# Kernel tuning notes

Hardware: AMD Instinct MI355X
Metric: run time of the kernel (lower is better)

## Reference

```python
import jax, jax.numpy as jnp
import numpy as np

V, H, B, T = 32000, 1024, 32, 256  # vocab, rnn_size, batch, seq_length


def setup_inputs() -> dict:
    key = jax.random.key(0)
    ks = jax.random.split(key, 6)
    s = 1.0 / np.sqrt(H)
    return {
        "input_data": jax.random.randint(ks[0], (B, T), 0, V, dtype=jnp.int32),
        "targets": jax.random.randint(ks[1], (B, T), 0, V, dtype=jnp.int32),
        "embedding": jax.random.uniform(ks[2], (V, H), minval=-1.0, maxval=1.0, dtype=jnp.float32),
        "softmax_b": jnp.zeros((V,), jnp.float32),
        "W0": (jax.random.normal(ks[3], (2 * H, 4 * H)) * s).astype(jnp.float32),
        "b0": jnp.zeros((4 * H,), jnp.float32),
        "W1": (jax.random.normal(ks[4], (2 * H, 4 * H)) * s).astype(jnp.float32),
        "b1": jnp.zeros((4 * H,), jnp.float32),
    }


def _lstm_step(x, c, h, W, b):
    # TF LSTMCell: gates i, j, f, o; forget_bias = 1.0
    z = jnp.concatenate([x, h], axis=-1) @ W + b  # [B, 4H]
    i, j, f, o = jnp.split(z, 4, axis=-1)
    c2 = c * jax.nn.sigmoid(f + 1.0) + jax.nn.sigmoid(i) * jnp.tanh(j)
    h2 = jax.nn.sigmoid(o) * jnp.tanh(c2)
    return c2, h2


def reference(input_data, targets, embedding, softmax_b, W0, b0, W1, b1):
    x = embedding[input_data]  # [B, T, H]
    Bb, Hh = x.shape[0], embedding.shape[1]
    zeros = jnp.zeros((Bb, Hh), x.dtype)
    init = ((zeros, zeros), (zeros, zeros))  # ((c0,h0),(c1,h1))

    def step(carry, xt):
        (c0, h0), (c1, h1) = carry
        c0, h0 = _lstm_step(xt, c0, h0, W0, b0)
        c1, h1 = _lstm_step(h0, c1, h1, W1, b1)
        return ((c0, h0), (c1, h1)), h1

    _, outs = jax.lax.scan(step, init, jnp.swapaxes(x, 0, 1))  # [T, B, H]
    output = jnp.swapaxes(outs, 0, 1).reshape(-1, Hh)  # [B*T, H]
    logits = output @ embedding.T + softmax_b  # tied softmax weights, [B*T, V]
    labels = targets.reshape(-1)
    logp = jax.nn.log_softmax(logits)
    loss = -jnp.take_along_axis(logp, labels[:, None], axis=1)[:, 0]
    cost = jnp.sum(loss) / Bb
    return logits, cost
```

## Files before the change

kernel.cpp:

```cpp
#include <hip/hip_runtime.h>
#include <hip/hip_bf16.h>

#define DEV static __device__ __forceinline__

typedef unsigned short u16;
typedef unsigned long long u64;
typedef __attribute__((ext_vector_type(8))) short short8;
typedef __attribute__((ext_vector_type(4))) float f32x4;

constexpr int V = 32000, H = 1024, B = 32, T = 256;
constexpr int BT = B * T;
constexpr int G  = 4 * H;
constexpr int NCH = V / 128;
constexpr int NWG2 = 256;
constexpr int RSTRIDE = 32 * 2048 + 2048;

constexpr size_t SZ_WT    = (size_t)G * 2048 * 2;
constexpr size_t OFF_W0T  = 0;
constexpr size_t OFF_W1T  = OFF_W0T + SZ_WT;
constexpr size_t OFF_EBF  = OFF_W1T + SZ_WT;
constexpr size_t OFF_XBF  = OFF_EBF + (size_t)V * H * 2;
constexpr size_t OFF_XP0  = OFF_XBF + (size_t)BT * H * 2;
constexpr size_t OFF_H1   = OFF_XP0 + (size_t)BT * G * 2;
constexpr size_t OFF_HSEQ = OFF_H1 + (size_t)BT * H * 2;
constexpr size_t SZ_HSEQ  = (size_t)(T + 2) * RSTRIDE * 2;
constexpr size_t OFF_SYNC = OFF_HSEQ + SZ_HSEQ;
constexpr size_t OFF_PMAX = OFF_SYNC + 8192;
constexpr size_t OFF_PSUM = OFF_PMAX + (size_t)BT * NCH * 4;
constexpr size_t OFF_LOSS = OFF_PSUM + (size_t)BT * NCH * 4;

DEV u16 f2bf(float x) {
  union { float f; unsigned int u; } v; v.f = x;
  unsigned int r = v.u + 0x7fffu + ((v.u >> 16) & 1u);
  return (u16)(r >> 16);
}
DEV float bf2f(u16 b) {
  union { unsigned int u; float f; } v; v.u = ((unsigned int)b) << 16;
  return v.f;
}
DEV float sigm(float x) { return 1.f / (1.f + expf(-x)); }

DEV void gload_lds16(const u16* g, u16* l) {
  __builtin_amdgcn_global_load_lds(
      (__attribute__((address_space(1))) void*)g,
      (__attribute__((address_space(3))) void*)l, 16, 0, 0);
}


__global__ void k_transpose_cvt(const float* __restrict__ in, u16* __restrict__ out,
                                int R, int C) {
  __shared__ float tile[32][33];
  int bc = blockIdx.x * 32, br = blockIdx.y * 32;
  int tx = threadIdx.x & 31, ty0 = threadIdx.x >> 5;
#pragma unroll
  for (int i = 0; i < 4; ++i) {
    int ty = ty0 + i * 8;
    tile[ty][tx] = in[(size_t)(br + ty) * C + bc + tx];
  }
  __syncthreads();
#pragma unroll
  for (int i = 0; i < 4; ++i) {
    int ty = ty0 + i * 8;
    out[(size_t)(bc + ty) * R + br + tx] = f2bf(tile[tx][ty]);
  }
}

__global__ void k_cvt_bf16(const float* __restrict__ in, u16* __restrict__ out, int n4) {
  int i = blockIdx.x * blockDim.x + threadIdx.x;
  int stride = gridDim.x * blockDim.x;
  for (; i < n4; i += stride) {
    float4 v = ((const float4*)in)[i];
    ushort4 o;
    o.x = f2bf(v.x); o.y = f2bf(v.y); o.z = f2bf(v.z); o.w = f2bf(v.w);
    ((ushort4*)out)[i] = o;
  }
}

__global__ void k_gather_x(const float* __restrict__ emb, const int* __restrict__ inp,
                           u16* __restrict__ Xbf) {
  int row = blockIdx.x;
  int t = row >> 5, b = row & 31;
  int tok = inp[b * T + t];
  const float4* src = (const float4*)(emb + (size_t)tok * H);
  ushort4* dst = (ushort4*)(Xbf + (size_t)row * H);
  float4 v = src[threadIdx.x];
  ushort4 o;
  o.x = f2bf(v.x); o.y = f2bf(v.y); o.z = f2bf(v.z); o.w = f2bf(v.w);
  dst[threadIdx.x] = o;
}

__global__ void k_zero(unsigned int* __restrict__ p, int nwords) {
  int i = blockIdx.x * blockDim.x + threadIdx.x;
  int stride = gridDim.x * blockDim.x;
  for (; i < nwords; i += stride) p[i] = 0u;
}

template <bool SM_EPI, int CMODE>
__global__ __launch_bounds__(256)
void k_gemm(const u16* __restrict__ A, int lda,
            const u16* __restrict__ Bt, int ldb,
            float* __restrict__ C, int ldc,
            const float* __restrict__ bias, int K,
            float* __restrict__ pmax, float* __restrict__ psum, int nch) {
  __shared__ alignas(16) u16 ldsA[128 * 32];
  __shared__ alignas(16) u16 ldsB[128 * 32];
  __shared__ float2 red[128][2];

  unsigned nwg = gridDim.x * gridDim.y;
  unsigned flat = blockIdx.y * gridDim.x + blockIdx.x;
  unsigned nf = (flat & 7) * (nwg >> 3) + (flat >> 3);
  unsigned bx = nf % gridDim.x, by = nf / gridDim.x;

  int tid = threadIdx.x, lane = tid & 63, w = tid >> 6;
  int row0 = by * 128, col0 = bx * 128;
  int wr = w >> 1, wc = w & 1;
  int c15 = lane & 15, q4 = lane >> 4;

  const u16* ag[2]; const u16* bg[2];
#pragma unroll
  for (int j = 0; j < 2; ++j) {
    int r = (j * 4 + w) * 16 + (lane >> 2);
    int k = (lane & 3) * 8;
    ag[j] = A + (size_t)(row0 + r) * lda + k;
    bg[j] = Bt + (size_t)(col0 + r) * ldb + k;
  }
  u16* lA0 = ldsA + (size_t)(0 + w) * 512;
  u16* lA1 = ldsA + (size_t)(4 + w) * 512;
  u16* lB0 = ldsB + (size_t)(0 + w) * 512;
  u16* lB1 = ldsB + (size_t)(4 + w) * 512;

  f32x4 acc[4][4];
#pragma unroll
  for (int m = 0; m < 4; ++m)
#pragma unroll
    for (int n = 0; n < 4; ++n) acc[m][n] = (f32x4){0.f, 0.f, 0.f, 0.f};

  int nk = K >> 5;
  for (int kk = 0; kk < nk; ++kk) {
    int kb = kk * 32;
    gload_lds16(ag[0] + kb, lA0);
    gload_lds16(ag[1] + kb, lA1);
    gload_lds16(bg[0] + kb, lB0);
    gload_lds16(bg[1] + kb, lB1);
    __syncthreads();

    short8 af[4], bfr[4];
#pragma unroll
    for (int m = 0; m < 4; ++m)
      af[m] = *(const short8*)(ldsA + (wr * 64 + m * 16 + c15) * 32 + q4 * 8);
#pragma unroll
    for (int n = 0; n < 4; ++n)
      bfr[n] = *(const short8*)(ldsB + (wc * 64 + n * 16 + c15) * 32 + q4 * 8);
#pragma unroll
    for (int m = 0; m < 4; ++m)
#pragma unroll
      for (int n = 0; n < 4; ++n)
        acc[m][n] = __builtin_amdgcn_mfma_f32_16x16x32_bf16(af[m], bfr[n], acc[m][n], 0, 0, 0);
    __syncthreads();
  }

  float bias_n[4];
#pragma unroll
  for (int n = 0; n < 4; ++n) bias_n[n] = bias[col0 + wc * 64 + n * 16 + c15];

#pragma unroll
  for (int m = 0; m < 4; ++m) {
#pragma unroll
    for (int jr = 0; jr < 4; ++jr) {
      int r_g = row0 + wr * 64 + m * 16 + q4 * 4 + jr;
      float v[4];
#pragma unroll
      for (int n = 0; n < 4; ++n) {
        int c_g = col0 + wc * 64 + n * 16 + c15;
        float val = acc[m][n][jr] + bias_n[n];
        if (CMODE == 0) {
          C[(size_t)r_g * ldc + c_g] = val;
        } else {
          int tt = r_g >> 5, bb = r_g & 31;
          int q = c_g >> 10, wgup = (c_g & 1023) >> 3, uu = c_g & 7;
          ((u16*)C)[((((size_t)tt * 128 + wgup) * 32 + bb) * 32) + q * 8 + uu] = f2bf(val);
        }
        v[n] = val;
      }
      if (SM_EPI) {
        float mx = fmaxf(fmaxf(v[0], v[1]), fmaxf(v[2], v[3]));
        float s = __expf(v[0] - mx) + __expf(v[1] - mx) + __expf(v[2] - mx) + __expf(v[3] - mx);
#pragma unroll
        for (int d = 1; d < 16; d <<= 1) {
          float mo = __shfl_xor(mx, d, 64);
          float so = __shfl_xor(s, d, 64);
          float M2 = fmaxf(mx, mo);
          s = s * __expf(mx - M2) + so * __expf(mo - M2);
          mx = M2;
        }
        if (c15 == 0) red[wr * 64 + m * 16 + q4 * 4 + jr][wc] = make_float2(mx, s);
      }
    }
  }
  if (SM_EPI) {
    __syncthreads();
    if (tid < 128) {
      float2 a = red[tid][0], b2 = red[tid][1];
      float M2 = fmaxf(a.x, b2.x);
      float S = a.y * __expf(a.x - M2) + b2.y * __expf(b2.x - M2);
      pmax[(size_t)(row0 + tid) * nch + bx] = M2;
      psum[(size_t)(row0 + tid) * nch + bx] = S;
    }
  }
}


#define RED(w_, bt_, nt_, r_, c_) red[((((w_)*2 + (bt_)) * 2 + (nt_)) * 16 + (r_)) * 16 + (c_)]

DEV void bar_sync(int* __restrict__ cnt, int target) {
  __syncthreads();
  if (threadIdx.x == 0) {
    __hip_atomic_fetch_add(cnt, 1, __ATOMIC_RELAXED, __HIP_MEMORY_SCOPE_AGENT);
    while (__hip_atomic_load(cnt, __ATOMIC_RELAXED, __HIP_MEMORY_SCOPE_AGENT) < target)
      __builtin_amdgcn_s_sleep(4);
  }
  __builtin_amdgcn_sched_barrier(0);
  __syncthreads();
}

DEV void epoch_wait(const int* __restrict__ cnt, int target) {
  if (threadIdx.x == 0) {
    while (__hip_atomic_load(cnt, __ATOMIC_RELAXED, __HIP_MEMORY_SCOPE_AGENT) < target)
      __builtin_amdgcn_s_sleep(4);
  }
  __builtin_amdgcn_sched_barrier(0);
  __syncthreads();
}

template <int KH, bool IS_L0>
DEV void lstm_role(const u16* __restrict__ WT,
                   const u16* __restrict__ xp0p,
                   const float* __restrict__ zb1,
                   u16* __restrict__ hseq, u16* __restrict__ H1bf,
                   int* __restrict__ c_own, int* __restrict__ c_epoch,
                   float* __restrict__ red, int wgu) {
  constexpr int KOFF = IS_L0 ? 1024 : 0;
  constexpr int KS = KH / 4;
  constexpr int NKC = KS / 32;
  int tid = threadIdx.x, lane = tid & 63, w = tid >> 6;
  int c15 = lane & 15, q4 = lane >> 4;
  int eb = tid >> 3, eu = tid & 7;

  short8 wfr[2][NKC];
#pragma unroll
  for (int nt = 0; nt < 2; ++nt) {
    int lr = nt * 16 + c15;
    const u16* rp = WT + (size_t)((lr >> 3) * 1024 + wgu * 8 + (lr & 7)) * 2048
                    + KOFF + w * KS + q4 * 8;
#pragma unroll
    for (int kc = 0; kc < NKC; ++kc)
      wfr[nt][kc] = *(const short8*)(rp + kc * 32);
  }

  float zpc[4];
  if (!IS_L0) {
#pragma unroll
    for (int q = 0; q < 4; ++q) zpc[q] = zb1[q * 1024 + wgu * 8 + eu];
  }
  float creg = 0.f;

  for (int it_t = 0; it_t < T; ++it_t) {
    int t = IS_L0 ? it_t : it_t + 1;

    if (!IS_L0) epoch_wait(c_epoch, 128 * t);

    float zp[4];
    if (IS_L0) {
#pragma unroll
      for (int q = 0; q < 4; ++q)
        zp[q] = bf2f(xp0p[((((size_t)t * 128 + wgu) * 32 + eb) * 32) + q * 8 + eu]);
    } else {
#pragma unroll
      for (int q = 0; q < 4; ++q) zp[q] = zpc[q];
    }

    const u16* hread = hseq + (size_t)t * RSTRIDE;
    f32x4 acc[2][2];
#pragma unroll
    for (int bt = 0; bt < 2; ++bt)
#pragma unroll
      for (int nt = 0; nt < 2; ++nt) acc[bt][nt] = (f32x4){0.f, 0.f, 0.f, 0.f};

#pragma unroll
    for (int kc = 0; kc < NKC; ++kc) {
      int kh = w * KS + kc * 32 + q4 * 8;
      short8 a0 = *(const short8*)(hread + (size_t)c15 * 2048 + kh);
      short8 a1 = *(const short8*)(hread + (size_t)(16 + c15) * 2048 + kh);
      acc[0][0] = __builtin_amdgcn_mfma_f32_16x16x32_bf16(a0, wfr[0][kc], acc[0][0], 0, 0, 0);
      acc[0][1] = __builtin_amdgcn_mfma_f32_16x16x32_bf16(a0, wfr[1][kc], acc[0][1], 0, 0, 0);
      acc[1][0] = __builtin_amdgcn_mfma_f32_16x16x32_bf16(a1, wfr[0][kc], acc[1][0], 0, 0, 0);
      acc[1][1] = __builtin_amdgcn_mfma_f32_16x16x32_bf16(a1, wfr[1][kc], acc[1][1], 0, 0, 0);
    }

#pragma unroll
    for (int bt = 0; bt < 2; ++bt)
#pragma unroll
      for (int nt = 0; nt < 2; ++nt)
#pragma unroll
        for (int jr = 0; jr < 4; ++jr)
          RED(w, bt, nt, q4 * 4 + jr, c15) = acc[bt][nt][jr];
    __syncthreads();

    int bt = eb >> 4, rr = eb & 15;
    float z[4];
#pragma unroll
    for (int q = 0; q < 4; ++q) {
      int lr = q * 8 + eu, nt = lr >> 4, cc = lr & 15;
      z[q] = RED(0, bt, nt, rr, cc) + RED(1, bt, nt, rr, cc) +
             RED(2, bt, nt, rr, cc) + RED(3, bt, nt, rr, cc) + zp[q];
    }
    float gi = sigm(z[0]);
    float gj = tanhf(z[1]);
    float gf = sigm(z[2] + 1.f);
    float go = sigm(z[3]);
    creg = creg * gf + gi * gj;
    float hv = go * tanhf(creg);

    int hb = (int)f2bf(hv);
    int hp = __shfl_xor(hb, 1, 64);
    if (!(tid & 1)) {
      unsigned int pack = (unsigned int)(u16)hb | ((unsigned int)(u16)hp << 16);
      u16* hwr = hseq + (size_t)(t + 1) * RSTRIDE + (IS_L0 ? 0 : 1024);
      __hip_atomic_store((unsigned int*)(hwr + (size_t)eb * 2048 + wgu * 8 + eu), pack,
                         __ATOMIC_RELAXED, __HIP_MEMORY_SCOPE_AGENT);
      if (!IS_L0)
        *(unsigned int*)(H1bf + ((size_t)eb * T + (t - 1)) * H + wgu * 8 + eu) = pack;
    }

    bar_sync(c_own, 128 * (IS_L0 ? t + 1 : t));
  }
}

__global__ __launch_bounds__(256, 1)
void k_lstm_persistent(const u16* __restrict__ W0T, const u16* __restrict__ W1T,
                       const u16* __restrict__ xp0p, const float* __restrict__ b1,
                       u16* __restrict__ hseq, u16* __restrict__ H1bf,
                       int* __restrict__ sync) {
  __shared__ float red[4 * 2 * 2 * 16 * 16];
  int wg = blockIdx.x;
  if (wg < 128)
    lstm_role<1024, true>(W0T, xp0p, nullptr, hseq, H1bf, sync, nullptr, red, wg);
  else
    lstm_role<2048, false>(W1T, nullptr, b1, hseq, H1bf, sync + 64, sync, red, wg - 128);
}

__global__ void k_rowfin(const float* __restrict__ pmax, const float* __restrict__ psum,
                         const float* __restrict__ Cl, const int* __restrict__ targets,
                         float* __restrict__ loss) {
  int row = blockIdx.x;
  int tid = threadIdx.x, lane = tid & 63, w = tid >> 6;
  float mx = -1e30f, s = 0.f;
  if (tid < NCH) { mx = pmax[(size_t)row * NCH + tid]; s = psum[(size_t)row * NCH + tid]; }
#pragma unroll
  for (int d = 1; d < 64; d <<= 1) {
    float mo = __shfl_xor(mx, d, 64);
    float so = __shfl_xor(s, d, 64);
    float M2 = fmaxf(mx, mo);
    s = s * __expf(mx - M2) + so * __expf(mo - M2);
    mx = M2;
  }
  __shared__ float2 wred[4];
  if (lane == 0) wred[w] = make_float2(mx, s);
  __syncthreads();
  if (tid == 0) {
    float M = wred[0].x, S = wred[0].y;
#pragma unroll
    for (int i = 1; i < 4; ++i) {
      float M2 = fmaxf(M, wred[i].x);
      S = S * __expf(M - M2) + wred[i].y * __expf(wred[i].x - M2);
      M = M2;
    }
    float logZ = M + logf(S);
    int tgt = targets[row];
    float xt = Cl[(size_t)row * V + tgt];
    loss[row] = logZ - xt;
  }
}

__global__ void k_cost(const float* __restrict__ loss, float* __restrict__ out) {
  int tid = threadIdx.x, lane = tid & 63, w = tid >> 6;
  float s = 0.f;
  for (int i = tid; i < BT; i += 256) s += loss[i];
#pragma unroll
  for (int d = 1; d < 64; d <<= 1) s += __shfl_xor(s, d, 64);
  __shared__ float ws4[4];
  if (lane == 0) ws4[w] = s;
  __syncthreads();
  if (tid == 0) out[0] = (ws4[0] + ws4[1] + ws4[2] + ws4[3]) * (1.0f / B);
}

extern "C" void kernel_launch(void* const* d_in, const int* in_sizes, int n_in,
                              void* d_out, int out_size, void* d_ws, size_t ws_size,
                              hipStream_t stream) {
  const int*   input_data = (const int*)d_in[0];
  const int*   targets    = (const int*)d_in[1];
  const float* emb        = (const float*)d_in[2];
  const float* softmax_b  = (const float*)d_in[3];
  const float* W0         = (const float*)d_in[4];
  const float* b0         = (const float*)d_in[5];
  const float* W1         = (const float*)d_in[6];
  const float* b1         = (const float*)d_in[7];
  float* out = (float*)d_out;
  char*  ws  = (char*)d_ws;

  u16*   W0T  = (u16*)(ws + OFF_W0T);
  u16*   W1T  = (u16*)(ws + OFF_W1T);
  u16*   Ebf  = (u16*)(ws + OFF_EBF);
  u16*   Xbf  = (u16*)(ws + OFF_XBF);
  u16*   xp0p = (u16*)(ws + OFF_XP0);
  u16*   H1bf = (u16*)(ws + OFF_H1);
  u16*   hseq = (u16*)(ws + OFF_HSEQ);
  int*   sync = (int*)(ws + OFF_SYNC);
  float* pmax = (float*)(ws + OFF_PMAX);
  float* psum = (float*)(ws + OFF_PSUM);
  float* lossb= (float*)(ws + OFF_LOSS);

  k_transpose_cvt<<<dim3(G / 32, 2048 / 32), 256, 0, stream>>>(W0, W0T, 2048, G);
  k_transpose_cvt<<<dim3(G / 32, 2048 / 32), 256, 0, stream>>>(W1, W1T, 2048, G);
  k_cvt_bf16<<<2048, 256, 0, stream>>>(emb, Ebf, V * H / 4);
  k_gather_x<<<BT, 256, 0, stream>>>(emb, input_data, Xbf);
  k_zero<<<64, 256, 0, stream>>>((unsigned int*)(ws + OFF_HSEQ), RSTRIDE);
  k_zero<<<1, 256, 0, stream>>>((unsigned int*)(ws + OFF_SYNC), 2048);

  k_gemm<false, 1><<<dim3(G / 128, BT / 128), 256, 0, stream>>>(
      Xbf, H, W0T, 2048, (float*)xp0p, G, b0, H, nullptr, nullptr, 0);

  k_lstm_persistent<<<dim3(NWG2), dim3(256), 0, stream>>>(
      W0T, W1T, xp0p, b1, hseq, H1bf, sync);

  k_gemm<true, 0><<<dim3(V / 128, BT / 128), 256, 0, stream>>>(
      H1bf, H, Ebf, H, out, V, softmax_b, H, pmax, psum, NCH);

  k_rowfin<<<BT, 256, 0, stream>>>(pmax, psum, out, targets, lossb);
  k_cost<<<1, 256, 0, stream>>>(lossb, out + (size_t)BT * V);
}
```

Baseline: 3.190 ms.

## Replace atomic counter barriers with per-timestep per-workgroup flag arrays in LSTM

Replaces the shared atomic-add counter barriers in the persistent LSTM kernel with per-timestep, per-workgroup ready flags. Each workgroup publishes its own flag with a plain store after writing h, and consumers poll 128 flags in parallel with one wavefront. Layer 1 now waits only on the layer-0 flags for step t-1 and its own layer's flags for t-2, which removes atomic contention on a single counter and loosens the layer coupling. The cost is a larger flag buffer that must be zeroed each run, and it relies on relaxed-ordering visibility of the h stores before the flag.

```diff
diff --git a/kernel.cpp b/kernel.cpp
--- a/kernel.cpp
+++ b/kernel.cpp
@@ -25,7 +25,8 @@
 constexpr size_t OFF_HSEQ = OFF_H1 + (size_t)BT * H * 2;
 constexpr size_t SZ_HSEQ  = (size_t)(T + 2) * RSTRIDE * 2;
 constexpr size_t OFF_SYNC = OFF_HSEQ + SZ_HSEQ;
-constexpr size_t OFF_PMAX = OFF_SYNC + 8192;
+constexpr size_t SZ_SYNC  = (size_t)2 * 256 * 128 * 4;
+constexpr size_t OFF_PMAX = OFF_SYNC + SZ_SYNC;
 constexpr size_t OFF_PSUM = OFF_PMAX + (size_t)BT * NCH * 4;
 constexpr size_t OFF_LOSS = OFF_PSUM + (size_t)BT * NCH * 4;
 
@@ -212,24 +213,33 @@
 
 #define RED(w_, bt_, nt_, r_, c_) red[((((w_)*2 + (bt_)) * 2 + (nt_)) * 16 + (r_)) * 16 + (c_)]
 
-DEV void bar_sync(int* __restrict__ cnt, int target) {
-  __syncthreads();
-  if (threadIdx.x == 0) {
-    __hip_atomic_fetch_add(cnt, 1, __ATOMIC_RELAXED, __HIP_MEMORY_SCOPE_AGENT);
-    while (__hip_atomic_load(cnt, __ATOMIC_RELAXED, __HIP_MEMORY_SCOPE_AGENT) < target)
-      __builtin_amdgcn_s_sleep(4);
+DEV void wait_flags(const int* __restrict__ fa, const int* __restrict__ fb) {
+  if (threadIdx.x < 64) {
+    int lane = threadIdx.x;
+    while (true) {
+      int ok = 1;
+      if (fa) {
+        int a0 = __hip_atomic_load(fa + lane,      __ATOMIC_RELAXED, __HIP_MEMORY_SCOPE_AGENT);
+        int a1 = __hip_atomic_load(fa + 64 + lane, __ATOMIC_RELAXED, __HIP_MEMORY_SCOPE_AGENT);
+        ok &= (a0 != 0) & (a1 != 0);
+      }
+      if (fb) {
+        int b0 = __hip_atomic_load(fb + lane,      __ATOMIC_RELAXED, __HIP_MEMORY_SCOPE_AGENT);
+        int b1 = __hip_atomic_load(fb + 64 + lane, __ATOMIC_RELAXED, __HIP_MEMORY_SCOPE_AGENT);
+        ok &= (b0 != 0) & (b1 != 0);
+      }
+      if (__all(ok)) break;
+      __builtin_amdgcn_s_sleep(2);
+    }
   }
   __builtin_amdgcn_sched_barrier(0);
   __syncthreads();
 }
 
-DEV void epoch_wait(const int* __restrict__ cnt, int target) {
-  if (threadIdx.x == 0) {
-    while (__hip_atomic_load(cnt, __ATOMIC_RELAXED, __HIP_MEMORY_SCOPE_AGENT) < target)
-      __builtin_amdgcn_s_sleep(4);
-  }
-  __builtin_amdgcn_sched_barrier(0);
+DEV void publish_flag(int* __restrict__ word) {
   __syncthreads();
+  if (threadIdx.x == 0)
+    __hip_atomic_store(word, 1, __ATOMIC_RELAXED, __HIP_MEMORY_SCOPE_AGENT);
 }
 
 template <int KH, bool IS_L0>
@@ -237,7 +247,7 @@
                    const u16* __restrict__ xp0p,
                    const float* __restrict__ zb1,
                    u16* __restrict__ hseq, u16* __restrict__ H1bf,
-                   int* __restrict__ c_own, int* __restrict__ c_epoch,
+                   int* __restrict__ f0, int* __restrict__ f1,
                    float* __restrict__ red, int wgu) {
   constexpr int KOFF = IS_L0 ? 1024 : 0;
   constexpr int KS = KH / 4;
@@ -267,8 +277,6 @@
   for (int it_t = 0; it_t < T; ++it_t) {
     int t = IS_L0 ? it_t : it_t + 1;
 
-    if (!IS_L0) epoch_wait(c_epoch, 128 * t);
-
     float zp[4];
     if (IS_L0) {
 #pragma unroll
@@ -277,6 +285,13 @@
     } else {
 #pragma unroll
       for (int q = 0; q < 4; ++q) zp[q] = zpc[q];
+    }
+
+    if (IS_L0) {
+      if (t >= 1) wait_flags(f0 + (size_t)(t - 1) * 128, nullptr);
+    } else {
+      wait_flags(f0 + (size_t)(t - 1) * 128,
+                 t >= 2 ? f1 + (size_t)(t - 2) * 128 : nullptr);
     }
 
     const u16* hread = hseq + (size_t)t * RSTRIDE;
@@ -332,7 +347,8 @@
         *(unsigned int*)(H1bf + ((size_t)eb * T + (t - 1)) * H + wgu * 8 + eu) = pack;
     }
 
-    bar_sync(c_own, 128 * (IS_L0 ? t + 1 : t));
+    publish_flag(IS_L0 ? (f0 + (size_t)t * 128 + wgu)
+                       : (f1 + (size_t)(t - 1) * 128 + wgu));
   }
 }
 
@@ -342,11 +358,13 @@
                        u16* __restrict__ hseq, u16* __restrict__ H1bf,
                        int* __restrict__ sync) {
   __shared__ float red[4 * 2 * 2 * 16 * 16];
+  int* f0 = sync;
+  int* f1 = sync + 256 * 128;
   int wg = blockIdx.x;
   if (wg < 128)
-    lstm_role<1024, true>(W0T, xp0p, nullptr, hseq, H1bf, sync, nullptr, red, wg);
+    lstm_role<1024, true>(W0T, xp0p, nullptr, hseq, H1bf, f0, f1, red, wg);
   else
-    lstm_role<2048, false>(W1T, nullptr, b1, hseq, H1bf, sync + 64, sync, red, wg - 128);
+    lstm_role<2048, false>(W1T, nullptr, b1, hseq, H1bf, f0, f1, red, wg - 128);
 }
 
 __global__ void k_rowfin(const float* __restrict__ pmax, const float* __restrict__ psum,
@@ -425,7 +443,7 @@
   k_cvt_bf16<<<2048, 256, 0, stream>>>(emb, Ebf, V * H / 4);
   k_gather_x<<<BT, 256, 0, stream>>>(emb, input_data, Xbf);
   k_zero<<<64, 256, 0, stream>>>((unsigned int*)(ws + OFF_HSEQ), RSTRIDE);
-  k_zero<<<1, 256, 0, stream>>>((unsigned int*)(ws + OFF_SYNC), 2048);
+  k_zero<<<64, 256, 0, stream>>>((unsigned int*)(ws + OFF_SYNC), (int)(SZ_SYNC / 4));
 
   k_gemm<false, 1><<<dim3(G / 128, BT / 128), 256, 0, stream>>>(
       Xbf, H, W0T, 2048, (float*)xp0p, G, b0, H, nullptr, nullptr, 0);
```

New measurement: 2.997 ms. 1.06x faster.
